# Kernel tuning notes

Measured on AMD Instinct MI355X. Metric: run time of the kernel, lower is better.

## Reference

```python
import jax, jax.numpy as jnp
import numpy as np

GELU = lambda v: jax.nn.gelu(v, approximate=False)  # torch nn.GELU default (exact erf)


def _gconv(x, w):
    # grouped conv1d, valid padding; w: (C,1,K), groups=C. lax conv = cross-correlation, same as torch.
    return jax.lax.conv_general_dilated(x, w, (1,), [(0, 0)],
                                        dimension_numbers=('NCH', 'OIH', 'NCH'),
                                        feature_group_count=x.shape[1])


def _conv(x, w, b):
    # dense conv1d, kernel 3, padding=1
    y = jax.lax.conv_general_dilated(x, w, (1,), [(1, 1)],
                                     dimension_numbers=('NCH', 'OIH', 'NCH'))
    return y + b[None, :, None]


def setup_inputs() -> dict:
    key = jax.random.key(0)
    ks = jax.random.split(key, 12)
    B, C, L = 8, 64, 2048
    H, FL, HD, TD, level = 32, 8, 64, 16, 3
    Cs = (1 + level) * C  # 256 channels into the ODE
    n = lambda k, s: (jax.random.normal(k, s) * 0.05).astype(jnp.float32)
    z = lambda s: jnp.zeros(s, jnp.float32)
    return dict(
        x=jax.random.normal(ks[0], (B, C, L), jnp.float32),
        # DyWAN_QR params
        sw1=n(ks[1], (H, C)), sb1=z((H,)),
        sw2=n(ks[2], (H, H)), sb2=z((H,)),
        sw3=n(ks[3], (2 * FL, H)), sb3=z((2 * FL,)),
        # ODE time embed / FiLM params
        tw1=n(ks[4], (TD, 1)), tb1=z((TD,)),
        tw2=n(ks[5], (TD, TD)), tb2=z((TD,)),
        cw=n(ks[6], (2 * HD, TD)), cb=z((2 * HD,)),
        # ODE conv stack params
        k1=n(ks[7], (HD, Cs, 3)), kb1=z((HD,)),
        k2=n(ks[8], (HD, HD, 3)), kb2=z((HD,)),
        k3=n(ks[9], (Cs, HD, 3)), kb3=z((Cs,)),
    )


def reference(x, sw1, sb1, sw2, sb2, sw3, sb3, tw1, tb1, tw2, tb2, cw, cb,
              k1, kb1, k2, kb2, k3, kb3):
    B, C, L = x.shape
    level, FL, T = 3, 8, 5

    def dywan(a):
        # stat_net: adaptive max pool over L -> (B,C) -> Linear -> GELU
        feat = GELU(jnp.max(a, axis=-1) @ sw1.T + sb1)
        raw = GELU(feat @ sw2.T + sb2) @ sw3.T + sb3  # (B, 2*FL)
        lo_raw, hi_raw = raw[:, :FL], raw[:, FL:]
        # QR of an (FL,1) column vector == L2 normalization (up to LAPACK sign)
        lo = lo_raw / jnp.linalg.norm(lo_raw, axis=1, keepdims=True)
        hi = hi_raw / jnp.linalg.norm(hi_raw, axis=1, keepdims=True)
        return lo, hi

    pad = FL - 1
    coeffs = [x]
    approx = x
    for _ in range(level):
        lo, hi = dywan(approx)
        lo_f = jnp.broadcast_to(lo.mean(0)[None, None, :], (C, 1, FL))
        hi_f = jnp.broadcast_to(hi.mean(0)[None, None, :], (C, 1, FL))
        ap = jnp.pad(approx, ((0, 0), (0, 0), (pad // 2, pad - pad // 2)), mode='reflect')
        new_approx = _gconv(ap, lo_f)[..., :L]
        coeffs.append(_gconv(ap, hi_f)[..., :L])
        approx = new_approx
    stacked = jnp.concatenate(coeffs, axis=1)  # (B, (1+level)*C, L)

    def ode_f(t, y):
        te = jnp.reshape(t, (1, 1)).astype(y.dtype)
        te = GELU(te @ tw1.T + tb1) @ tw2.T + tb2          # (1, TD)
        cond = te @ cw.T + cb                               # (1, 2*HD)
        hd = cond.shape[1] // 2
        gamma, beta = cond[:, :hd], cond[:, hd:]
        h = _conv(y, k1, kb1)
        h = (1.0 + gamma[:, :, None]) * h + beta[:, :, None]  # FiLM
        h = GELU(h)
        h = GELU(_conv(h, k2, kb2))
        return _conv(h, k3, kb3)

    # dopri5 tableau, fixed grid over linspace(0, 1, T) (b7 = 0, so 6 stages)
    hs = 1.0 / (T - 1)
    y = stacked
    for i in range(T - 1):
        t0 = i * hs
        s1 = ode_f(t0, y)
        s2 = ode_f(t0 + hs / 5, y + hs * (1 / 5) * s1)
        s3 = ode_f(t0 + 3 * hs / 10, y + hs * (3 / 40 * s1 + 9 / 40 * s2))
        s4 = ode_f(t0 + 4 * hs / 5, y + hs * (44 / 45 * s1 - 56 / 15 * s2 + 32 / 9 * s3))
        s5 = ode_f(t0 + 8 * hs / 9, y + hs * (19372 / 6561 * s1 - 25360 / 2187 * s2
                                              + 64448 / 6561 * s3 - 212 / 729 * s4))
        s6 = ode_f(t0 + hs, y + hs * (9017 / 3168 * s1 - 355 / 33 * s2 + 46732 / 5247 * s3
                                      + 49 / 176 * s4 - 5103 / 18656 * s5))
        y = y + hs * (35 / 384 * s1 + 500 / 1113 * s3 + 125 / 192 * s4
                      - 2187 / 6784 * s5 + 11 / 84 * s6)
    ode_out = y

    yl = ode_out[:, :C, :]
    yh0 = ode_out[:, C:2 * C, :]
    yh1 = ode_out[:, 2 * C:3 * C, :]
    yh2 = ode_out[:, 3 * C:4 * C, :]

    dx = ode_f(jnp.float32(1.0), ode_out)
    inner = jnp.sum(stacked * dx, axis=(1, 2))  # (B,)
    ecloss = jnp.mean(inner ** 2)
    return (yl, yh0, yh1, yh2, ecloss)
```

## Files before the change

### kernel.cpp

```cpp
#include <hip/hip_runtime.h>
#include <math.h>

#define B 8
#define C 64
#define L 2048
#define CS 256
#define BCL  (B*C*L)
#define BCSL (B*CS*L)
#define HS 0.25f

typedef unsigned short u16;
typedef unsigned int   u32;
typedef __attribute__((ext_vector_type(8))) short sh8;
typedef __attribute__((ext_vector_type(4))) float f4;
typedef __attribute__((ext_vector_type(8))) unsigned short us8;
typedef __attribute__((ext_vector_type(4))) unsigned short us4;

__device__ __forceinline__ float gelu(float x) {
    return 0.5f * x * (1.0f + erff(x * 0.70710678118654752440f));
}
__device__ __forceinline__ u16 f2b(float f) {
    u32 u = __float_as_uint(f);
    u32 r = u + 0x7FFFu + ((u >> 16) & 1u);
    return (u16)(r >> 16);
}
__device__ __forceinline__ float b2f(u16 h) {
    return __uint_as_float(((u32)h) << 16);
}
__device__ __forceinline__ u32 encmax(float f) {
    u32 b = __float_as_uint(f);
    return (b & 0x80000000u) ? ~b : (b | 0x80000000u);
}
__device__ __forceinline__ float decmax(u32 u) {
    return __uint_as_float((u & 0x80000000u) ? (u ^ 0x80000000u) : ~u);
}

struct ComboB { const u16* p[6]; float c[6]; };

__global__ __launch_bounds__(256) void prep_k(const float* __restrict__ w,
        u16* __restrict__ dst, int IC, int OC) {
    int idx = blockIdx.x * 256 + threadIdx.x;
    int OCG = OC >> 4;
    int j = idx & 7, lane = (idx >> 3) & 63, t = idx >> 9;
    int ocg = t % OCG, c = t / OCG;
    int oc = ocg * 16 + (lane & 15);
    int K = c * 32 + ((lane >> 4) & 3) * 8 + j;
    int kk = K / IC, ic = K % IC;
    dst[idx] = f2b(w[((size_t)oc * IC + ic) * 3 + kk]);
}

__global__ void cond25_k(const float* __restrict__ tw1, const float* __restrict__ tb1,
                         const float* __restrict__ tw2, const float* __restrict__ tb2,
                         const float* __restrict__ cw, const float* __restrict__ cb,
                         float* __restrict__ condall) {
    __shared__ float te1[16], te2[16];
    int tix = blockIdx.x;
    int tid = threadIdx.x;
    double add[6] = {0.0, 0.25/5.0, 3.0*0.25/10.0, 4.0*0.25/5.0, 8.0*0.25/9.0, 0.25};
    float t = (tix == 24) ? 1.0f : (float)((double)(tix / 6) * 0.25 + add[tix % 6]);
    if (tid < 16) te1[tid] = gelu(t * tw1[tid] + tb1[tid]);
    __syncthreads();
    if (tid < 16) {
        float s = tb2[tid];
        for (int k = 0; k < 16; ++k) s += te1[k] * tw2[tid*16+k];
        te2[tid] = s;
    }
    __syncthreads();
    float s = cb[tid];
    for (int j = 0; j < 16; ++j) s += te2[j] * cw[tid*16+j];
    condall[tix*128 + tid] = s;
}

template<int NC, int EPI>
__global__ __launch_bounds__(512) void fused_k(ComboB in,
        const u16* __restrict__ wp1, const float* __restrict__ kb1,
        const u16* __restrict__ wp2, const float* __restrict__ kb2,
        const u16* __restrict__ wp3, const float* __restrict__ kb3,
        const float* __restrict__ condall, int tix,
        u16* __restrict__ outSb,
        float* __restrict__ y, u16* __restrict__ yb,
        float* __restrict__ outp, const float* __restrict__ stacked,
        double* __restrict__ inner)
{
    __shared__ u16 xs1[50][264];
    __shared__ u16 h1t[50][72];
    __shared__ u16 h2t[34][72];
    __shared__ u16 ypart[32][264];
    __shared__ double sred[8];
    const int tid = threadIdx.x;
    const int l0  = blockIdx.x * 32;
    const int b   = blockIdx.y;
    const int g0  = l0 - 3;

    const float cy1 = HS*(35.f/384.f), cy3 = HS*(500.f/1113.f),
                cy4 = HS*(125.f/192.f), cy5 = -HS*(2187.f/6784.f),
                cy6 = HS*(11.f/84.f);

    for (int i = tid; i < 12*264; i += 512) xs1[38 + i/264][i%264] = 0;
    if (tid < 144) h1t[48 + tid/72][tid%72] = 0;

    for (int idx = tid; idx < 38*32; idx += 512) {
        int r = idx >> 5, c8 = idx & 31;
        int gl = g0 + r;
        us8 val;
        if (gl >= 0 && gl < L) {
            size_t a = ((size_t)b * L + gl) * 256 + c8 * 8;
            us8 v0 = *(const us8*)(in.p[0] + a);
            if (NC == 1) {
                val = v0;
            } else {
                float f[8];
                float yp[8];
                #pragma unroll
                for (int j = 0; j < 8; ++j) { f[j] = b2f(v0[j]); yp[j] = 0.f; }
                #pragma unroll
                for (int t = 1; t < NC; ++t) {
                    us8 vt = *(const us8*)(in.p[t] + a);
                    #pragma unroll
                    for (int j = 0; j < 8; ++j) {
                        float bv = b2f(vt[j]);
                        f[j] += in.c[t] * bv;
                        if ((EPI == 1 || EPI == 2) && (t == 1 || t == 3 || t == 4 || t == 5)) {
                            float cy = (t == 1) ? cy1 : (t == 3) ? cy3 : (t == 4) ? cy4 : cy5;
                            yp[j] += cy * bv;
                        }
                    }
                }
                #pragma unroll
                for (int j = 0; j < 8; ++j) val[j] = f2b(f[j]);
                if ((EPI == 1 || EPI == 2) && r >= 3 && r < 35) {
                    us8 ypk;
                    #pragma unroll
                    for (int j = 0; j < 8; ++j) ypk[j] = f2b(yp[j]);
                    *(us8*)&ypart[r - 3][c8 * 8] = ypk;
                }
            }
        } else {
            #pragma unroll
            for (int j = 0; j < 8; ++j) val[j] = 0;
        }
        *(us8*)&xs1[r][c8 * 8] = val;
    }
    __syncthreads();

    const int wave = tid >> 6, lane = tid & 63;
    const int nlo = lane & 15, quad = lane >> 4;

    const int ocg12  = wave & 3;
    const int nfbase = (wave < 4) ? 0 : 2;
    const int nfcnt  = (wave < 4) ? 2 : 1;

    f4 a1[2];
    a1[0] = f4{0.f,0.f,0.f,0.f}; a1[1] = a1[0];
    {
        const sh8* w1 = (const sh8*)wp1;
        for (int c = 0; c < 24; ++c) {
            int kk = c >> 3, ic0 = (c & 7) << 5;
            sh8 A = w1[(c*4 + ocg12)*64 + lane];
            #pragma unroll
            for (int k = 0; k < 2; ++k) {
                if (k < nfcnt) {
                    int nf = nfbase + k;
                    sh8 Bv = *(const sh8*)&xs1[nf*16 + nlo + kk][ic0 + quad*8];
                    a1[k] = __builtin_amdgcn_mfma_f32_16x16x32_bf16(A, Bv, a1[k], 0, 0, 0);
                }
            }
        }
    }
    {
        const float* cd = condall + tix*128;
        const int oc0 = ocg12*16 + quad*4;
        #pragma unroll
        for (int k = 0; k < 2; ++k) {
            if (k < nfcnt) {
                int nf = nfbase + k;
                int p = nf*16 + nlo;
                int gp = l0 - 2 + p;
                bool ok = (p < 36) && (gp >= 0) && (gp < L);
                us4 pk;
                #pragma unroll
                for (int reg = 0; reg < 4; ++reg) {
                    int oc = oc0 + reg;
                    float v = (1.f + cd[oc]) * (a1[k][reg] + kb1[oc]) + cd[64+oc];
                    pk[reg] = ok ? f2b(gelu(v)) : (u16)0;
                }
                *(us4*)&h1t[p][oc0] = pk;
            }
        }
    }
    __syncthreads();

    f4 a2[2];
    a2[0] = f4{0.f,0.f,0.f,0.f}; a2[1] = a2[0];
    {
        const sh8* w2 = (const sh8*)wp2;
        #pragma unroll
        for (int c = 0; c < 6; ++c) {
            int kk = c >> 1, ic0 = (c & 1) << 5;
            sh8 A = w2[(c*4 + ocg12)*64 + lane];
            #pragma unroll
            for (int k = 0; k < 2; ++k) {
                if (k < nfcnt) {
                    int nf = nfbase + k;
                    sh8 Bv = *(const sh8*)&h1t[nf*16 + nlo + kk][ic0 + quad*8];
                    a2[k] = __builtin_amdgcn_mfma_f32_16x16x32_bf16(A, Bv, a2[k], 0, 0, 0);
                }
            }
        }
    }
    {
        const int oc0 = ocg12*16 + quad*4;
        #pragma unroll
        for (int k = 0; k < 2; ++k) {
            if (k < nfcnt) {
                int nf = nfbase + k;
                int q = nf*16 + nlo;
                if (q < 34) {
                    int gq = l0 - 1 + q;
                    bool ok = (gq >= 0) && (gq < L);
                    us4 pk;
                    #pragma unroll
                    for (int reg = 0; reg < 4; ++reg)
                        pk[reg] = ok ? f2b(gelu(a2[k][reg] + kb2[oc0 + reg])) : (u16)0;
                    *(us4*)&h2t[q][oc0] = pk;
                }
            }
        }
    }
    __syncthreads();

    f4 a3[2][2];
    #pragma unroll
    for (int mf = 0; mf < 2; ++mf) { a3[mf][0] = f4{0.f,0.f,0.f,0.f}; a3[mf][1] = a3[mf][0]; }
    {
        const sh8* w3 = (const sh8*)wp3;
        #pragma unroll
        for (int c = 0; c < 6; ++c) {
            int kk = c >> 1, ic0 = (c & 1) << 5;
            sh8 B0 = *(const sh8*)&h2t[nlo + kk][ic0 + quad*8];
            sh8 B1 = *(const sh8*)&h2t[16 + nlo + kk][ic0 + quad*8];
            #pragma unroll
            for (int mf = 0; mf < 2; ++mf) {
                sh8 A = w3[(c*16 + wave*2 + mf)*64 + lane];
                a3[mf][0] = __builtin_amdgcn_mfma_f32_16x16x32_bf16(A, B0, a3[mf][0], 0, 0, 0);
                a3[mf][1] = __builtin_amdgcn_mfma_f32_16x16x32_bf16(A, B1, a3[mf][1], 0, 0, 0);
            }
        }
    }

    if (EPI == 3) {
        double acc = 0.0;
        #pragma unroll
        for (int mf = 0; mf < 2; ++mf)
            #pragma unroll
            for (int nf = 0; nf < 2; ++nf) {
                int pos = l0 + nf*16 + nlo;
                #pragma unroll
                for (int reg = 0; reg < 4; ++reg) {
                    int oc = (wave*2 + mf)*16 + quad*4 + reg;
                    size_t idx = ((size_t)b*CS + oc)*L + pos;
                    float dx = a3[mf][nf][reg] + kb3[oc];
                    acc += (double)stacked[idx] * (double)dx;
                }
            }
        #pragma unroll
        for (int off = 32; off > 0; off >>= 1) acc += __shfl_down(acc, off, 64);
        if (lane == 0) sred[wave] = acc;
        __syncthreads();
        if (tid == 0) {
            double s = 0.0;
            #pragma unroll
            for (int w = 0; w < 8; ++w) s += sred[w];
            atomicAdd(&inner[b], s);
        }
    } else if (EPI == 0) {
        #pragma unroll
        for (int mf = 0; mf < 2; ++mf) {
            int baseoc = (wave*2 + mf)*16 + quad*4;
            #pragma unroll
            for (int nf = 0; nf < 2; ++nf) {
                int pos = l0 + nf*16 + nlo;
                us4 pk;
                #pragma unroll
                for (int reg = 0; reg < 4; ++reg)
                    pk[reg] = f2b(a3[mf][nf][reg] + kb3[baseoc + reg]);
                *(us4*)(outSb + ((size_t)b*L + pos)*256 + baseoc) = pk;
            }
        }
    } else {
        #pragma unroll
        for (int mf = 0; mf < 2; ++mf) {
            int baseoc = (wave*2 + mf)*16 + quad*4;
            #pragma unroll
            for (int nf = 0; nf < 2; ++nf) {
                int pl = nf*16 + nlo;
                int pos = l0 + pl;
                us4 yp4 = *(const us4*)&ypart[pl][baseoc];
                us4 pk;
                #pragma unroll
                for (int reg = 0; reg < 4; ++reg) {
                    int oc = baseoc + reg;
                    size_t idx = ((size_t)b*CS + oc)*L + pos;
                    float s6 = a3[mf][nf][reg] + kb3[oc];
                    float yv = y[idx] + b2f(yp4[reg]) + cy6 * s6;
                    pk[reg] = f2b(yv);
                    if (EPI == 1) y[idx] = yv;
                    if (EPI == 2) {
                        size_t oidx = (((size_t)(oc >> 6)*B + b)*64 + (oc & 63))*L + pos;
                        outp[oidx] = yv;
                    }
                }
                *(us4*)(yb + ((size_t)b*L + pos)*256 + baseoc) = pk;
            }
        }
    }
}

__global__ __launch_bounds__(256) void mlp_k(const u32* __restrict__ bm,
    const float* __restrict__ sw1, const float* __restrict__ sb1,
    const float* __restrict__ sw2, const float* __restrict__ sb2,
    const float* __restrict__ sw3, const float* __restrict__ sb3,
    float* __restrict__ filt) {
    __shared__ float m[8][64], f1[8][32], f2[8][32], raw[8][16], nrm[8][2];
    int tid = threadIdx.x;
    for (int i = tid; i < 512; i += 256) m[i >> 6][i & 63] = decmax(bm[i]);
    __syncthreads();
    {
        int b = tid >> 5, h = tid & 31;
        float s = sb1[h];
        for (int c = 0; c < 64; ++c) s += m[b][c] * sw1[h*64+c];
        f1[b][h] = gelu(s);
    }
    __syncthreads();
    {
        int b = tid >> 5, h = tid & 31;
        float s = sb2[h];
        for (int k = 0; k < 32; ++k) s += f1[b][k] * sw2[h*32+k];
        f2[b][h] = gelu(s);
    }
    __syncthreads();
    if (tid < 128) {
        int b = tid >> 4, j = tid & 15;
        float s = sb3[j];
        for (int k = 0; k < 32; ++k) s += f2[b][k] * sw3[j*32+k];
        raw[b][j] = s;
    }
    __syncthreads();
    if (tid < 16) {
        int b = tid >> 1, half = tid & 1;
        float s = 0.f;
        for (int j = 0; j < 8; ++j) { float v = raw[b][half*8+j]; s += v*v; }
        nrm[b][half] = sqrtf(s);
    }
    __syncthreads();
    if (tid < 16) {
        int half = tid >> 3;
        float s = 0.f;
        for (int b = 0; b < 8; ++b) s += raw[b][tid] / nrm[b][half];
        filt[tid] = s * 0.125f;
    }
}

__global__ __launch_bounds__(256) void wconv_k(const float* __restrict__ ap,
    const float* __restrict__ filt, float* __restrict__ apOut,
    float* __restrict__ stacked, int lev, u32* __restrict__ bmaxn) {
    __shared__ float f[16];
    __shared__ float red[256];
    if (threadIdx.x < 16) f[threadIdx.x] = filt[threadIdx.x];
    __syncthreads();
    size_t idx = (size_t)blockIdx.x * 256 + threadIdx.x;
    int l = (int)(idx & 2047);
    size_t bc = idx >> 11;
    int c = (int)(bc & 63), b = (int)(bc >> 6);
    const float* row = ap + (bc << 11);
    float lo = 0.f, hi = 0.f;
    #pragma unroll
    for (int k = 0; k < 8; ++k) {
        int mI = l + k - 3;
        mI = mI < 0 ? -mI : (mI >= L ? 2*L - 2 - mI : mI);
        float v = row[mI];
        lo += v * f[k];
        hi += v * f[8+k];
    }
    stacked[((size_t)b * CS + (size_t)(lev+1) * 64 + c) * L + l] = hi;
    if (bmaxn) {
        apOut[idx] = lo;
        red[threadIdx.x] = lo;
        __syncthreads();
        for (int s = 128; s > 0; s >>= 1) {
            if (threadIdx.x < s) red[threadIdx.x] = fmaxf(red[threadIdx.x], red[threadIdx.x + s]);
            __syncthreads();
        }
        if (threadIdx.x == 0) atomicMax(&bmaxn[blockIdx.x >> 3], encmax(red[0]));
    }
}

__global__ __launch_bounds__(256) void copyx_k(const float* __restrict__ x,
        float* __restrict__ st, u32* __restrict__ bmax0) {
    __shared__ float red[256];
    size_t i = (size_t)blockIdx.x * 256 + threadIdx.x;
    size_t b = i >> 17, rem = i & 131071;
    float v = x[i];
    st[b * ((size_t)CS*L) + rem] = v;
    red[threadIdx.x] = v;
    __syncthreads();
    for (int s = 128; s > 0; s >>= 1) {
        if (threadIdx.x < s) red[threadIdx.x] = fmaxf(red[threadIdx.x], red[threadIdx.x + s]);
        __syncthreads();
    }
    if (threadIdx.x == 0) atomicMax(&bmax0[blockIdx.x >> 3], encmax(red[0]));
}

__global__ __launch_bounds__(256) void tinit_k(const float* __restrict__ st,
        float* __restrict__ y, u16* __restrict__ yb) {
    __shared__ float t[64][65];
    const int tid = threadIdx.x;
    const int l0 = blockIdx.x * 64, c0 = blockIdx.y * 64, b = blockIdx.z;
    #pragma unroll
    for (int k = 0; k < 16; ++k) {
        int c = k * 4 + (tid >> 6), l = tid & 63;
        size_t idx = ((size_t)b*CS + c0 + c) * L + l0 + l;
        float v = st[idx];
        y[idx] = v;
        t[c][l] = v;
    }
    __syncthreads();
    #pragma unroll
    for (int k = 0; k < 16; ++k) {
        int p = k * 4 + (tid >> 6), ch = tid & 63;
        yb[((size_t)b * L + l0 + p) * 256 + c0 + ch] = f2b(t[ch][p]);
    }
}

__global__ void ecfin_k(const double* __restrict__ inner, float* __restrict__ out) {
    double s = 0.0;
    for (int b = 0; b < 8; ++b) s += inner[b] * inner[b];
    out[BCSL] = (float)(s / 8.0);
}

extern "C" void kernel_launch(void* const* d_in, const int* in_sizes, int n_in,
                              void* d_out, int out_size, void* d_ws, size_t ws_size,
                              hipStream_t stream) {
    const float* x   = (const float*)d_in[0];
    const float* sw1 = (const float*)d_in[1];
    const float* sb1 = (const float*)d_in[2];
    const float* sw2 = (const float*)d_in[3];
    const float* sb2 = (const float*)d_in[4];
    const float* sw3 = (const float*)d_in[5];
    const float* sb3 = (const float*)d_in[6];
    const float* tw1 = (const float*)d_in[7];
    const float* tb1 = (const float*)d_in[8];
    const float* tw2 = (const float*)d_in[9];
    const float* tb2 = (const float*)d_in[10];
    const float* cw  = (const float*)d_in[11];
    const float* cb  = (const float*)d_in[12];
    const float* k1  = (const float*)d_in[13];
    const float* kb1 = (const float*)d_in[14];
    const float* k2  = (const float*)d_in[15];
    const float* kb2 = (const float*)d_in[16];
    const float* k3  = (const float*)d_in[17];
    const float* kb3 = (const float*)d_in[18];
    float* out = (float*)d_out;

    char* cur = (char*)d_ws;
    auto alloc = [&](size_t bytes) { void* p = cur; cur += (bytes + 255) & ~(size_t)255; return p; };
    float* stacked = (float*)alloc(BCSL * 4);
    float* y       = (float*)alloc(BCSL * 4);
    u16*   yb      = (u16*)  alloc(BCSL * 2);
    u16*   sbuf[5];
    for (int i = 0; i < 5; ++i) sbuf[i] = (u16*)alloc(BCSL * 2);
    float* cond  = (float*)alloc(3200 * 4);
    double* inner = (double*)alloc(8 * 8);
    u32* bmaxe   = (u32*)alloc(3 * 512 * 4);
    float* filt  = (float*)alloc(16 * 4);
    u16* wp1 = (u16*)alloc(49152 * 2);
    u16* wp2 = (u16*)alloc(12288 * 2);
    u16* wp3 = (u16*)alloc(49152 * 2);

    u16 *s1b = sbuf[0], *s2b = sbuf[1], *s3b = sbuf[2], *s4b = sbuf[3], *s5b = sbuf[4];

    hipMemsetAsync(inner, 0, 256 + 3 * 512 * 4, stream);

    prep_k<<<192, 256, 0, stream>>>(k1, wp1, CS, C);
    prep_k<<<48,  256, 0, stream>>>(k2, wp2, C,  C);
    prep_k<<<192, 256, 0, stream>>>(k3, wp3, C,  CS);
    cond25_k<<<25, 128, 0, stream>>>(tw1, tb1, tw2, tb2, cw, cb, cond);

    copyx_k<<<4096, 256, 0, stream>>>(x, stacked, bmaxe);
    const float* apIn = x;
    float* apBuf[2] = {(float*)s1b, (float*)s2b};
    for (int lev = 0; lev < 3; ++lev) {
        mlp_k<<<1, 256, 0, stream>>>(bmaxe + lev*512, sw1, sb1, sw2, sb2, sw3, sb3, filt);
        float* apOut = apBuf[lev & 1];
        wconv_k<<<4096, 256, 0, stream>>>(apIn, filt, apOut, stacked, lev,
                                          (lev < 2) ? (bmaxe + (lev+1)*512) : nullptr);
        apIn = apOut;
    }
    tinit_k<<<dim3(32, 4, 8), 256, 0, stream>>>(stacked, y, yb);

    const float hs = HS;
    dim3 cg(64, 8);
    #define LAUNCH(NC, EPI, CIN, TIX, OUTSB, OUTP, STK) \
        fused_k<NC, EPI><<<cg, 512, 0, stream>>>(CIN, wp1, kb1, wp2, kb2, wp3, kb3, \
            cond, TIX, OUTSB, y, yb, OUTP, STK, inner)

    for (int i = 0; i < 4; ++i) {
        ComboB cA{}; cA.p[0] = yb;
        LAUNCH(1, 0, cA, i*6+0, s1b, nullptr, nullptr);

        ComboB cB{}; cB.p[0] = yb; cB.p[1] = s1b; cB.c[1] = hs*(1.f/5.f);
        LAUNCH(2, 0, cB, i*6+1, s2b, nullptr, nullptr);

        ComboB cC{}; cC.p[0] = yb;
        cC.p[1] = s1b; cC.c[1] = hs*(3.f/40.f);
        cC.p[2] = s2b; cC.c[2] = hs*(9.f/40.f);
        LAUNCH(3, 0, cC, i*6+2, s3b, nullptr, nullptr);

        ComboB cD{}; cD.p[0] = yb;
        cD.p[1] = s1b; cD.c[1] = hs*(44.f/45.f);
        cD.p[2] = s2b; cD.c[2] = -hs*(56.f/15.f);
        cD.p[3] = s3b; cD.c[3] = hs*(32.f/9.f);
        LAUNCH(4, 0, cD, i*6+3, s4b, nullptr, nullptr);

        ComboB cE{}; cE.p[0] = yb;
        cE.p[1] = s1b; cE.c[1] = hs*(19372.f/6561.f);
        cE.p[2] = s2b; cE.c[2] = -hs*(25360.f/2187.f);
        cE.p[3] = s3b; cE.c[3] = hs*(64448.f/6561.f);
        cE.p[4] = s4b; cE.c[4] = -hs*(212.f/729.f);
        LAUNCH(5, 0, cE, i*6+4, s5b, nullptr, nullptr);

        ComboB cF{}; cF.p[0] = yb;
        cF.p[1] = s1b; cF.c[1] = hs*(9017.f/3168.f);
        cF.p[2] = s2b; cF.c[2] = -hs*(355.f/33.f);
        cF.p[3] = s3b; cF.c[3] = hs*(46732.f/5247.f);
        cF.p[4] = s4b; cF.c[4] = hs*(49.f/176.f);
        cF.p[5] = s5b; cF.c[5] = -hs*(5103.f/18656.f);
        if (i < 3) {
            LAUNCH(6, 1, cF, i*6+5, nullptr, nullptr, nullptr);
        } else {
            LAUNCH(6, 2, cF, i*6+5, nullptr, out, nullptr);
        }
    }

    ComboB cZ{}; cZ.p[0] = yb;
    LAUNCH(1, 3, cZ, 24, nullptr, nullptr, stacked);
    ecfin_k<<<1, 1, 0, stream>>>(inner, out);
    #undef LAUNCH
}
```

Baseline: 696.0 us.

## Prefetch MFMA weight fragments into registers and double-buffer the bf16 state

```diff
diff --git a/kernel.cpp b/kernel.cpp
--- a/kernel.cpp
+++ b/kernel.cpp
@@ -36,6 +36,12 @@
 }
 
 struct ComboB { const u16* p[6]; float c[6]; };
+
+__device__ __forceinline__ void ldw_a6(const sh8* __restrict__ w, int cb, int g,
+                                       int lane, sh8 (&A)[6]) {
+    #pragma unroll
+    for (int u = 0; u < 6; ++u) A[u] = w[((cb + u)*4 + g)*64 + lane];
+}
 
 __global__ __launch_bounds__(256) void prep_k(const float* __restrict__ w,
         u16* __restrict__ dst, int IC, int OC) {
@@ -72,13 +78,13 @@
 }
 
 template<int NC, int EPI>
-__global__ __launch_bounds__(512) void fused_k(ComboB in,
+__global__ __launch_bounds__(512, 4) void fused_k(ComboB in,
         const u16* __restrict__ wp1, const float* __restrict__ kb1,
         const u16* __restrict__ wp2, const float* __restrict__ kb2,
         const u16* __restrict__ wp3, const float* __restrict__ kb3,
         const float* __restrict__ condall, int tix,
         u16* __restrict__ outSb,
-        float* __restrict__ y, u16* __restrict__ yb,
+        float* __restrict__ y, u16* __restrict__ ybout,
         float* __restrict__ outp, const float* __restrict__ stacked,
         double* __restrict__ inner)
 {
@@ -96,6 +102,15 @@
                 cy4 = HS*(125.f/192.f), cy5 = -HS*(2187.f/6784.f),
                 cy6 = HS*(11.f/84.f);
 
+    const int wave = tid >> 6, lane = tid & 63;
+    const int nlo = lane & 15, quad = lane >> 4;
+    const int ocg12  = wave & 3;
+    const int nfbase = (wave < 4) ? 0 : 2;
+    const int nfcnt  = (wave < 4) ? 2 : 1;
+    const sh8* w1v = (const sh8*)wp1;
+    const sh8* w2v = (const sh8*)wp2;
+    const sh8* w3v = (const sh8*)wp3;
+
     for (int i = tid; i < 12*264; i += 512) xs1[38 + i/264][i%264] = 0;
     if (tid < 144) h1t[48 + tid/72][tid%72] = 0;
 
@@ -141,32 +156,39 @@
         }
         *(us8*)&xs1[r][c8 * 8] = val;
     }
-    __syncthreads();
-
-    const int wave = tid >> 6, lane = tid & 63;
-    const int nlo = lane & 15, quad = lane >> 4;
-
-    const int ocg12  = wave & 3;
-    const int nfbase = (wave < 4) ? 0 : 2;
-    const int nfcnt  = (wave < 4) ? 2 : 1;
+
+    sh8 A1a[6], A1b[6];
+    ldw_a6(w1v, 0, ocg12, lane, A1a);
+    __syncthreads();
 
     f4 a1[2];
     a1[0] = f4{0.f,0.f,0.f,0.f}; a1[1] = a1[0];
-    {
-        const sh8* w1 = (const sh8*)wp1;
-        for (int c = 0; c < 24; ++c) {
-            int kk = c >> 3, ic0 = (c & 7) << 5;
-            sh8 A = w1[(c*4 + ocg12)*64 + lane];
-            #pragma unroll
-            for (int k = 0; k < 2; ++k) {
-                if (k < nfcnt) {
-                    int nf = nfbase + k;
-                    sh8 Bv = *(const sh8*)&xs1[nf*16 + nlo + kk][ic0 + quad*8];
-                    a1[k] = __builtin_amdgcn_mfma_f32_16x16x32_bf16(A, Bv, a1[k], 0, 0, 0);
-                }
-            }
-        }
-    }
+    #define C1CHUNK(AA, CB)                                                          \
+    {                                                                                \
+        _Pragma("unroll")                                                            \
+        for (int u_ = 0; u_ < 6; ++u_) {                                             \
+            const int c_ = (CB) + u_;                                                \
+            const int kk_ = c_ >> 3, ic0_ = (c_ & 7) << 5;                           \
+            _Pragma("unroll")                                                        \
+            for (int k_ = 0; k_ < 2; ++k_) {                                         \
+                if (k_ < nfcnt) {                                                    \
+                    const int nf_ = nfbase + k_;                                     \
+                    sh8 Bv_ = *(const sh8*)&xs1[nf_*16 + nlo + kk_][ic0_ + quad*8];  \
+                    a1[k_] = __builtin_amdgcn_mfma_f32_16x16x32_bf16(AA[u_], Bv_, a1[k_], 0, 0, 0); \
+                }                                                                    \
+            }                                                                        \
+        }                                                                            \
+    }
+    ldw_a6(w1v, 6, ocg12, lane, A1b);
+    C1CHUNK(A1a, 0);
+    ldw_a6(w1v, 12, ocg12, lane, A1a);
+    C1CHUNK(A1b, 6);
+    ldw_a6(w1v, 18, ocg12, lane, A1b);
+    C1CHUNK(A1a, 12);
+    sh8 A2[6];
+    ldw_a6(w2v, 0, ocg12, lane, A2);
+    C1CHUNK(A1b, 18);
+    #undef C1CHUNK
     {
         const float* cd = condall + tix*128;
         const int oc0 = ocg12*16 + quad*4;
@@ -193,20 +215,24 @@
     f4 a2[2];
     a2[0] = f4{0.f,0.f,0.f,0.f}; a2[1] = a2[0];
     {
-        const sh8* w2 = (const sh8*)wp2;
         #pragma unroll
         for (int c = 0; c < 6; ++c) {
             int kk = c >> 1, ic0 = (c & 1) << 5;
-            sh8 A = w2[(c*4 + ocg12)*64 + lane];
             #pragma unroll
             for (int k = 0; k < 2; ++k) {
                 if (k < nfcnt) {
                     int nf = nfbase + k;
                     sh8 Bv = *(const sh8*)&h1t[nf*16 + nlo + kk][ic0 + quad*8];
-                    a2[k] = __builtin_amdgcn_mfma_f32_16x16x32_bf16(A, Bv, a2[k], 0, 0, 0);
-                }
-            }
-        }
+                    a2[k] = __builtin_amdgcn_mfma_f32_16x16x32_bf16(A2[c], Bv, a2[k], 0, 0, 0);
+                }
+            }
+        }
+    }
+    sh8 A3[12];
+    #pragma unroll
+    for (int i = 0; i < 12; ++i) {
+        int c = i >> 1, mf = i & 1;
+        A3[i] = w3v[(c*16 + wave*2 + mf)*64 + lane];
     }
     {
         const int oc0 = ocg12*16 + quad*4;
@@ -233,7 +259,6 @@
     #pragma unroll
     for (int mf = 0; mf < 2; ++mf) { a3[mf][0] = f4{0.f,0.f,0.f,0.f}; a3[mf][1] = a3[mf][0]; }
     {
-        const sh8* w3 = (const sh8*)wp3;
         #pragma unroll
         for (int c = 0; c < 6; ++c) {
             int kk = c >> 1, ic0 = (c & 1) << 5;
@@ -241,9 +266,8 @@
             sh8 B1 = *(const sh8*)&h2t[16 + nlo + kk][ic0 + quad*8];
             #pragma unroll
             for (int mf = 0; mf < 2; ++mf) {
-                sh8 A = w3[(c*16 + wave*2 + mf)*64 + lane];
-                a3[mf][0] = __builtin_amdgcn_mfma_f32_16x16x32_bf16(A, B0, a3[mf][0], 0, 0, 0);
-                a3[mf][1] = __builtin_amdgcn_mfma_f32_16x16x32_bf16(A, B1, a3[mf][1], 0, 0, 0);
+                a3[mf][0] = __builtin_amdgcn_mfma_f32_16x16x32_bf16(A3[c*2+mf], B0, a3[mf][0], 0, 0, 0);
+                a3[mf][1] = __builtin_amdgcn_mfma_f32_16x16x32_bf16(A3[c*2+mf], B1, a3[mf][1], 0, 0, 0);
             }
         }
     }
@@ -310,7 +334,7 @@
                         outp[oidx] = yv;
                     }
                 }
-                *(us4*)(yb + ((size_t)b*L + pos)*256 + baseoc) = pk;
+                *(us4*)(ybout + ((size_t)b*L + pos)*256 + baseoc) = pk;
             }
         }
     }
@@ -466,7 +490,8 @@
     auto alloc = [&](size_t bytes) { void* p = cur; cur += (bytes + 255) & ~(size_t)255; return p; };
     float* stacked = (float*)alloc(BCSL * 4);
     float* y       = (float*)alloc(BCSL * 4);
-    u16*   yb      = (u16*)  alloc(BCSL * 2);
+    u16*   yba     = (u16*)  alloc(BCSL * 2);
+    u16*   ybb     = (u16*)  alloc(BCSL * 2);
     u16*   sbuf[5];
     for (int i = 0; i < 5; ++i) sbuf[i] = (u16*)alloc(BCSL * 2);
     float* cond  = (float*)alloc(3200 * 4);
@@ -496,54 +521,58 @@
                                           (lev < 2) ? (bmaxe + (lev+1)*512) : nullptr);
         apIn = apOut;
     }
-    tinit_k<<<dim3(32, 4, 8), 256, 0, stream>>>(stacked, y, yb);
+    tinit_k<<<dim3(32, 4, 8), 256, 0, stream>>>(stacked, y, yba);
 
     const float hs = HS;
     dim3 cg(64, 8);
-    #define LAUNCH(NC, EPI, CIN, TIX, OUTSB, OUTP, STK) \
+    #define LAUNCH(NC, EPI, CIN, TIX, OUTSB, YBW, OUTP, STK) \
         fused_k<NC, EPI><<<cg, 512, 0, stream>>>(CIN, wp1, kb1, wp2, kb2, wp3, kb3, \
-            cond, TIX, OUTSB, y, yb, OUTP, STK, inner)
-
+            cond, TIX, OUTSB, y, YBW, OUTP, STK, inner)
+
+    u16* ybs[2] = {yba, ybb};
     for (int i = 0; i < 4; ++i) {
-        ComboB cA{}; cA.p[0] = yb;
-        LAUNCH(1, 0, cA, i*6+0, s1b, nullptr, nullptr);
-
-        ComboB cB{}; cB.p[0] = yb; cB.p[1] = s1b; cB.c[1] = hs*(1.f/5.f);
-        LAUNCH(2, 0, cB, i*6+1, s2b, nullptr, nullptr);
-
-        ComboB cC{}; cC.p[0] = yb;
+        u16* ybr = ybs[i & 1];
+        u16* ybw = ybs[(i & 1) ^ 1];
+
+        ComboB cA{}; cA.p[0] = ybr;
+        LAUNCH(1, 0, cA, i*6+0, s1b, nullptr, nullptr, nullptr);
+
+        ComboB cB{}; cB.p[0] = ybr; cB.p[1] = s1b; cB.c[1] = hs*(1.f/5.f);
+        LAUNCH(2, 0, cB, i*6+1, s2b, nullptr, nullptr, nullptr);
+
+        ComboB cC{}; cC.p[0] = ybr;
         cC.p[1] = s1b; cC.c[1] = hs*(3.f/40.f);
         cC.p[2] = s2b; cC.c[2] = hs*(9.f/40.f);
-        LAUNCH(3, 0, cC, i*6+2, s3b, nullptr, nullptr);
-
-        ComboB cD{}; cD.p[0] = yb;
+        LAUNCH(3, 0, cC, i*6+2, s3b, nullptr, nullptr, nullptr);
+
+        ComboB cD{}; cD.p[0] = ybr;
         cD.p[1] = s1b; cD.c[1] = hs*(44.f/45.f);
         cD.p[2] = s2b; cD.c[2] = -hs*(56.f/15.f);
         cD.p[3] = s3b; cD.c[3] = hs*(32.f/9.f);
-        LAUNCH(4, 0, cD, i*6+3, s4b, nullptr, nullptr);
-
-        ComboB cE{}; cE.p[0] = yb;
+        LAUNCH(4, 0, cD, i*6+3, s4b, nullptr, nullptr, nullptr);
+
+        ComboB cE{}; cE.p[0] = ybr;
         cE.p[1] = s1b; cE.c[1] = hs*(19372.f/6561.f);
         cE.p[2] = s2b; cE.c[2] = -hs*(25360.f/2187.f);
         cE.p[3] = s3b; cE.c[3] = hs*(64448.f/6561.f);
         cE.p[4] = s4b; cE.c[4] = -hs*(212.f/729.f);
-        LAUNCH(5, 0, cE, i*6+4, s5b, nullptr, nullptr);
-
-        ComboB cF{}; cF.p[0] = yb;
+        LAUNCH(5, 0, cE, i*6+4, s5b, nullptr, nullptr, nullptr);
+
+        ComboB cF{}; cF.p[0] = ybr;
         cF.p[1] = s1b; cF.c[1] = hs*(9017.f/3168.f);
         cF.p[2] = s2b; cF.c[2] = -hs*(355.f/33.f);
         cF.p[3] = s3b; cF.c[3] = hs*(46732.f/5247.f);
         cF.p[4] = s4b; cF.c[4] = hs*(49.f/176.f);
         cF.p[5] = s5b; cF.c[5] = -hs*(5103.f/18656.f);
         if (i < 3) {
-            LAUNCH(6, 1, cF, i*6+5, nullptr, nullptr, nullptr);
+            LAUNCH(6, 1, cF, i*6+5, nullptr, ybw, nullptr, nullptr);
         } else {
-            LAUNCH(6, 2, cF, i*6+5, nullptr, out, nullptr);
-        }
-    }
-
-    ComboB cZ{}; cZ.p[0] = yb;
-    LAUNCH(1, 3, cZ, 24, nullptr, nullptr, stacked);
+            LAUNCH(6, 2, cF, i*6+5, nullptr, ybw, out, nullptr);
+        }
+    }
+
+    ComboB cZ{}; cZ.p[0] = ybs[0];
+    LAUNCH(1, 3, cZ, 24, nullptr, nullptr, nullptr, stacked);
     ecfin_k<<<1, 1, 0, stream>>>(inner, out);
     #undef LAUNCH
 }
```

Result: faster. 642.8 us, median of 4 (-7.6%).
